# Kernel optimization log

Measured on AMD Instinct MI355X. Metric: run time of the kernel, lower is better.

The kernel has to match this reference:

```python
import jax, jax.numpy as jnp
import numpy as np
from jax import lax

EPS = 1e-5
KH, KW, PAD, DIL = 3, 3, 1, 1


def _bilinear_gather(x, py, px):
    """x: [B,C,H,W]; py/px: [B,K,H,W] float sample coords. Returns [B,C,K,H,W].
    Zero-padding semantics (torchvision deform_conv2d): corners outside the image contribute 0."""
    B, C, H, W = x.shape
    K = py.shape[1]
    y0 = jnp.floor(py)
    x0 = jnp.floor(px)
    wy1 = py - y0
    wy0 = 1.0 - wy1
    wx1 = px - x0
    wx0 = 1.0 - wx1
    xf = x.reshape(B, C, H * W)

    def corner(yc, xc, w):
        valid = (yc >= 0) & (yc <= H - 1) & (xc >= 0) & (xc <= W - 1)
        yi = jnp.clip(yc, 0, H - 1).astype(jnp.int32)
        xi = jnp.clip(xc, 0, W - 1).astype(jnp.int32)
        lin = (yi * W + xi).reshape(B, -1)  # [B, K*H*W]
        v = jax.vmap(lambda xb, lb: xb[:, lb])(xf, lin)  # [B, C, K*H*W]
        return v * (w * valid.astype(x.dtype)).reshape(B, 1, -1)

    out = (corner(y0, x0, wy0 * wx0)
           + corner(y0, x0 + 1.0, wy0 * wx1)
           + corner(y0 + 1.0, x0, wy1 * wx0)
           + corner(y0 + 1.0, x0 + 1.0, wy1 * wx1))
    return out.reshape(B, C, K, H, W)


def _deform_conv(x, offset, w):
    B, C, H, W = x.shape
    K = KH * KW
    off = offset.reshape(B, K, 2, H, W)  # (dy, dx) per kernel tap
    ki = (jnp.arange(K) // KW - PAD).astype(x.dtype)  # kernel row offset (dil=1)
    kj = (jnp.arange(K) % KW - PAD).astype(x.dtype)
    hh = jnp.arange(H).astype(x.dtype)
    ww = jnp.arange(W).astype(x.dtype)
    py = hh[None, None, :, None] + ki[None, :, None, None] + off[:, :, 0]
    px = ww[None, None, None, :] + kj[None, :, None, None] + off[:, :, 1]
    val = _bilinear_gather(x, py, px)  # [B,C,K,H,W]
    return jnp.einsum('bckhw,ock->bohw', val, w.reshape(w.shape[0], C, K))


def _bn(x, gamma, beta, mean, var):
    inv = gamma * lax.rsqrt(var + EPS)
    return x * inv[None, :, None, None] + (beta - mean * inv)[None, :, None, None]


def setup_inputs() -> dict:
    key = jax.random.key(0)
    ks = jax.random.split(key, 12)
    B, C, H, W = 4, 128, 128, 128
    return {
        'x': jax.random.normal(ks[0], (B, C, H, W), jnp.float32),
        'offset': jax.random.normal(ks[1], (B, 2 * KH * KW, H, W), jnp.float32),
        'w1': jax.random.normal(ks[2], (C, C, KH, KW), jnp.float32) * 0.05,
        'bn1_gamma': jax.random.uniform(ks[3], (C,), jnp.float32, 0.5, 1.5),
        'bn1_beta': jax.random.normal(ks[4], (C,), jnp.float32) * 0.1,
        'bn1_mean': jax.random.normal(ks[5], (C,), jnp.float32) * 0.1,
        'bn1_var': jax.random.uniform(ks[6], (C,), jnp.float32, 0.5, 1.5),
        'w2': jax.random.normal(ks[7], (C, C, KH, KW), jnp.float32) * 0.05,
        'bn2_gamma': jax.random.uniform(ks[8], (C,), jnp.float32, 0.5, 1.5),
        'bn2_beta': jax.random.normal(ks[9], (C,), jnp.float32) * 0.1,
        'bn2_mean': jax.random.normal(ks[10], (C,), jnp.float32) * 0.1,
        'bn2_var': jax.random.uniform(ks[11], (C,), jnp.float32, 0.5, 1.5),
    }


def reference(x, offset, w1, bn1_gamma, bn1_beta, bn1_mean, bn1_var,
              w2, bn2_gamma, bn2_beta, bn2_mean, bn2_var):
    identity = x
    out = _deform_conv(x, offset, w1)
    out = jax.nn.relu(_bn(out, bn1_gamma, bn1_beta, bn1_mean, bn1_var))
    out = lax.conv_general_dilated(out, w2, window_strides=(1, 1),
                                   padding=((PAD, PAD), (PAD, PAD)),
                                   dimension_numbers=('NCHW', 'OIHW', 'NCHW'))
    out = _bn(out, bn2_gamma, bn2_beta, bn2_mean, bn2_var)
    out = jax.nn.relu(out + identity)
    return out
```

## Files before the change

### kernel.cpp

```cpp
#include <hip/hip_runtime.h>
#include <hip/hip_fp16.h>
#include <stdint.h>

#define B_ 4
#define C_ 128
#define H_ 128
#define W_ 128
#define HW 16384

typedef _Float16 h8 __attribute__((ext_vector_type(8)));
typedef float f32x16 __attribute__((ext_vector_type(16)));

__device__ __forceinline__ unsigned cvtpk_f16(float lo, float hi) {
    auto r = __builtin_amdgcn_cvt_pkrtz(lo, hi);
    return *(unsigned*)&r;
}

__device__ __forceinline__ unsigned blend_h2(unsigned c0, unsigned c1, unsigned c2, unsigned c3,
                                             __half2 G0, __half2 G1, __half2 G2, __half2 G3) {
    __half2 s = __hmul2(G0, *(__half2*)&c0);
    s = __hfma2(G1, *(__half2*)&c1, s);
    s = __hfma2(G2, *(__half2*)&c2, s);
    s = __hfma2(G3, *(__half2*)&c3, s);
    return *(unsigned*)&s;
}

__device__ __forceinline__ void gll16(const void* g, void* l) {
    __builtin_amdgcn_global_load_lds((const unsigned int*)g, (unsigned int*)l, 16, 0, 0);
}

__global__ __launch_bounds__(256) void prep_all(const float* __restrict__ w1,
                                                const float* __restrict__ w2,
                                                unsigned short* __restrict__ w1f,
                                                unsigned short* __restrict__ w2t,
                                                unsigned short* __restrict__ o1p,
                                                const float* g1, const float* b1, const float* m1, const float* v1,
                                                const float* g2, const float* b2, const float* m2, const float* v2,
                                                float* inv1, float* sh1, float* inv2, float* sh2) {
    int blk = blockIdx.x;
    int tid = threadIdx.x;
    if (blk < 1152) {
        int i = blk * 256 + tid;
        if (i < 147456) {
            int o = i / 1152, rem = i % 1152;
            int c = rem / 9, tap = rem % 9;
            _Float16 hv = (_Float16)w1[i];
            int s = o >> 5;
            int ks = c >> 4;
            int l = (o & 31) | (((c >> 3) & 1) << 5);
            int jj = c & 7;
            w1f[(((tap * 4 + s) * 8 + ks) * 64 + l) * 8 + jj] = *(unsigned short*)&hv;
        } else {
            int j = i - 147456;
            int o = j / 1152, rem = j % 1152;
            int c = rem / 9, tap = rem % 9;
            _Float16 hv = (_Float16)w2[j];
            w2t[o * 1152 + tap * 128 + c] = *(unsigned short*)&hv;
        }
    } else if (blk < 1281) {
        int i = (blk - 1152) * 256 + tid;
        if (i < 33024) {
            int chunk = i & 15;
            int pos = i >> 4;
            int b = pos / 516;
            int r = pos % 516;
            int row, col;
            if (r < 130)      { row = 0;   col = r; }
            else if (r < 260) { row = 129; col = r - 130; }
            else { int j = r - 260; row = 1 + (j >> 1); col = (j & 1) * 129; }
            uint4 z = {0u, 0u, 0u, 0u};
            *(uint4*)((char*)o1p + (size_t)((b * 130 + row) * 130 + col) * 256 + chunk * 16) = z;
        }
    } else {
        if (tid < 128) {
            float iv = g1[tid] * rsqrtf(v1[tid] + 1e-5f);
            inv1[tid] = iv; sh1[tid] = b1[tid] - m1[tid] * iv;
        } else {
            int u = tid - 128;
            float iv = g2[u] * rsqrtf(v2[u] + 1e-5f);
            inv2[u] = iv; sh2[u] = b2[u] - m2[u] * iv;
        }
    }
}

__global__ __launch_bounds__(256) void nhwc_k(const float* __restrict__ x,
                                              unsigned short* __restrict__ xh) {
    __shared__ unsigned short tile[32][36];
    int blk = blockIdx.x;
    int wt = blk & 3, ct = (blk >> 2) & 3, h = (blk >> 4) & 127, b = blk >> 11;
    int t = threadIdx.x;
    int c = t >> 3, seg = t & 7;
    const float* srcp = x + ((size_t)((b * 128 + ct * 32 + c) * 128 + h) * 128) + wt * 32 + seg * 4;
    float4 v = *(const float4*)srcp;
    uint2 pk;
    pk.x = cvtpk_f16(v.x, v.y);
    pk.y = cvtpk_f16(v.z, v.w);
    *(uint2*)&tile[c][seg * 4] = pk;
    __syncthreads();
    int w = t >> 3, s2 = t & 7;
    unsigned a0 = tile[s2 * 4 + 0][w];
    unsigned a1 = tile[s2 * 4 + 1][w];
    unsigned a2 = tile[s2 * 4 + 2][w];
    unsigned a3 = tile[s2 * 4 + 3][w];
    uint2 o;
    o.x = (a1 << 16) | a0;
    o.y = (a3 << 16) | a2;
    *(uint2*)(xh + ((size_t)((b * 128 + h) * 128 + wt * 32 + w) * 128) + ct * 32 + s2 * 4) = o;
}

__global__ __launch_bounds__(512, 4) void gemm1_k(
    const unsigned short* __restrict__ xh,
    const float* __restrict__ off,
    const unsigned short* __restrict__ w1f,
    const float* __restrict__ inv1,
    const float* __restrict__ sh1,
    unsigned short* __restrict__ out1p) {
    __shared__ __align__(16) char ldsv[2][16384];

    int bid = blockIdx.x;
    int swz = ((bid & 7) << 7) | (bid >> 3);
    int half = swz & 1, h = (swz >> 1) & 127, b = swz >> 8;
    int w0 = half * 64;
    int tid = threadIdx.x;
    int bH = b * H_;
    const char* xb8 = (const char*)xh;

    if (tid < 256) {
        int prow = tid >> 4;
        int seg = tid & 15;
        int sb = seg * 16;

        float dy[4], dx[4];
        unsigned PX[4][4];
        float g[4][4];
        uint4 buf[2][4];

#define OFFLOAD(TT) do { \
    int dyB_ = ((b * 18 + 2 * (TT)) * H_ + h) * W_ + w0; \
    _Pragma("unroll") \
    for (int c_ = 0; c_ < 4; ++c_) { \
        int p_ = prow + c_ * 16; \
        dy[c_] = off[dyB_ + p_]; \
        dx[c_] = off[dyB_ + HW + p_]; \
    } \
} while (0)

#define COORD(TT) do { \
    int kh_ = (TT) / 3 - 1, kw_ = (TT) % 3 - 1; \
    _Pragma("unroll") \
    for (int c_ = 0; c_ < 4; ++c_) { \
        int p_ = prow + c_ * 16; \
        float py_ = (float)(h + kh_) + dy[c_]; \
        float px_ = (float)(w0 + p_ + kw_) + dx[c_]; \
        float y0f_ = floorf(py_), x0f_ = floorf(px_); \
        int y0_ = (int)y0f_, x0_ = (int)x0f_; \
        float wy1_ = py_ - y0f_, wx1_ = px_ - x0f_; \
        float wy0_ = 1.f - wy1_, wx0_ = 1.f - wx1_; \
        int y1_ = y0_ + 1, x1_ = x0_ + 1; \
        g[c_][0] = ((unsigned)y0_ < 128u && (unsigned)x0_ < 128u) ? wy0_ * wx0_ : 0.f; \
        g[c_][1] = ((unsigned)y0_ < 128u && (unsigned)x1_ < 128u) ? wy0_ * wx1_ : 0.f; \
        g[c_][2] = ((unsigned)y1_ < 128u && (unsigned)x0_ < 128u) ? wy1_ * wx0_ : 0.f; \
        g[c_][3] = ((unsigned)y1_ < 128u && (unsigned)x1_ < 128u) ? wy1_ * wx1_ : 0.f; \
        int y0c_ = min(max(y0_, 0), 127), y1c_ = min(max(y1_, 0), 127); \
        int x0c_ = min(max(x0_, 0), 127), x1c_ = min(max(x1_, 0), 127); \
        int r0_ = (bH + y0c_) * W_, r1_ = (bH + y1c_) * W_; \
        PX[c_][0] = (unsigned)((r0_ + x0c_) * 256) + sb; \
        PX[c_][1] = (unsigned)((r0_ + x1c_) * 256) + sb; \
        PX[c_][2] = (unsigned)((r1_ + x0c_) * 256) + sb; \
        PX[c_][3] = (unsigned)((r1_ + x1c_) * 256) + sb; \
    } \
} while (0)

#define ISSUE2(cA, cB) do { \
    _Pragma("unroll") \
    for (int k_ = 0; k_ < 4; ++k_) buf[0][k_] = *(const uint4*)(xb8 + PX[cA][k_]); \
    _Pragma("unroll") \
    for (int k_ = 0; k_ < 4; ++k_) buf[1][k_] = *(const uint4*)(xb8 + PX[cB][k_]); \
} while (0)

#define BLEND1(VP, CC, BI) do { \
    __half2 G0_ = __float2half2_rn(g[CC][0]); \
    __half2 G1_ = __float2half2_rn(g[CC][1]); \
    __half2 G2_ = __float2half2_rn(g[CC][2]); \
    __half2 G3_ = __float2half2_rn(g[CC][3]); \
    uint4 st_; \
    st_.x = blend_h2(buf[BI][0].x, buf[BI][1].x, buf[BI][2].x, buf[BI][3].x, G0_, G1_, G2_, G3_); \
    st_.y = blend_h2(buf[BI][0].y, buf[BI][1].y, buf[BI][2].y, buf[BI][3].y, G0_, G1_, G2_, G3_); \
    st_.z = blend_h2(buf[BI][0].z, buf[BI][1].z, buf[BI][2].z, buf[BI][3].z, G0_, G1_, G2_, G3_); \
    st_.w = blend_h2(buf[BI][0].w, buf[BI][1].w, buf[BI][2].w, buf[BI][3].w, G0_, G1_, G2_, G3_); \
    int row_ = prow + (CC) * 16; \
    *(uint4*)(&ldsv[VP][0] + row_ * 256 + ((seg ^ (row_ & 15)) << 4)) = st_; \
} while (0)

#define GATHER(VP) do { \
    ISSUE2(0, 1); \
    BLEND1(VP, 0, 0); BLEND1(VP, 1, 1); \
    ISSUE2(2, 3); \
    BLEND1(VP, 2, 0); BLEND1(VP, 3, 1); \
} while (0)

        OFFLOAD(0);
        COORD(0);
        GATHER(0);
        OFFLOAD(1);
        __syncthreads();
        for (int t = 0; t < 9; ++t) {
            if (t < 8) {
                COORD(t + 1);
                GATHER((t + 1) & 1);
                if (t < 7) OFFLOAD(t + 2);
            }
            __syncthreads();
        }
#undef OFFLOAD
#undef COORD
#undef ISSUE2
#undef BLEND1
#undef GATHER
    } else {
        int ctid = tid - 256;
        int lane = ctid & 63, wv2 = ctid >> 6;
        int wo = wv2 >> 1, wp = wv2 & 1;
        int lp = lane & 31, hi = lane >> 5;
        int bRow = (wp * 32 + lp) * 256;
        int lsw = lp & 15;

        f32x16 acc0 = {};
        f32x16 acc1 = {};

        __syncthreads();
        for (int t = 0; t < 9; ++t) {
            const unsigned short* wb = w1f + (t * 4 + 2 * wo) * 4096 + lane * 8;
            const char* vcur = &ldsv[t & 1][0];
            #pragma unroll 2
            for (int ks = 0; ks < 8; ++ks) {
                h8 a0 = *(const h8*)(wb + ks * 512);
                h8 a1 = *(const h8*)(wb + 4096 + ks * 512);
                int q0 = 2 * ks + hi;
                h8 bb = *(const h8*)(vcur + bRow + ((q0 ^ lsw) << 4));
                acc0 = __builtin_amdgcn_mfma_f32_32x32x16_f16(a0, bb, acc0, 0, 0, 0);
                acc1 = __builtin_amdgcn_mfma_f32_32x32x16_f16(a1, bb, acc1, 0, 0, 0);
            }
            __syncthreads();
        }

        int p = w0 + wp * 32 + lp;
        size_t rowbase = (size_t)((b * 130 + h + 1) * 130 + 1 + p) * 128;
        #pragma unroll
        for (int t = 0; t < 2; ++t) {
            #pragma unroll
            for (int k = 0; k < 4; ++k) {
                int o0 = wo * 64 + t * 32 + k * 8 + hi * 4;
                float4 iv = *(const float4*)(inv1 + o0);
                float4 sv = *(const float4*)(sh1 + o0);
                float e0, e1, e2, e3;
                if (t == 0) {
                    e0 = acc0[4 * k + 0]; e1 = acc0[4 * k + 1];
                    e2 = acc0[4 * k + 2]; e3 = acc0[4 * k + 3];
                } else {
                    e0 = acc1[4 * k + 0]; e1 = acc1[4 * k + 1];
                    e2 = acc1[4 * k + 2]; e3 = acc1[4 * k + 3];
                }
                float v0 = fmaxf(fmaf(e0, iv.x, sv.x), 0.f);
                float v1 = fmaxf(fmaf(e1, iv.y, sv.y), 0.f);
                float v2 = fmaxf(fmaf(e2, iv.z, sv.z), 0.f);
                float v3 = fmaxf(fmaf(e3, iv.w, sv.w), 0.f);
                uint2 pk2;
                pk2.x = cvtpk_f16(v0, v1);
                pk2.y = cvtpk_f16(v2, v3);
                *(uint2*)(out1p + rowbase + o0) = pk2;
            }
        }
    }
}

__global__ __launch_bounds__(512, 4) void gemm2_k(
    const unsigned short* __restrict__ out1p,
    const unsigned short* __restrict__ w2t,
    const unsigned short* __restrict__ xh,
    const float* __restrict__ inv2,
    const float* __restrict__ sh2,
    float* __restrict__ outp) {
    __shared__ __align__(16) char ldsS[33280];
    __shared__ __align__(16) char ldsw[32768];

    int bid = blockIdx.x;
    int swz = ((bid & 7) << 6) | (bid >> 3);
    int h = swz & 127, b = swz >> 7;
    int tid = threadIdx.x, lane = tid & 63, wv = tid >> 6;
    int wo = wv >> 2, wp = wv & 3;
    int lp = lane & 31, hi = lane >> 5;

    f32x16 acc0 = {};
    f32x16 acc1 = {};

    int aRow0 = (wo * 64 + lp) * 256;
    int aRow1 = aRow0 + 32 * 256;
    int lsw = lp & 15;

    for (int kh = 0; kh < 3; ++kh) {
        __syncthreads();
        const char* srow = (const char*)out1p + (size_t)((b * 130 + h + kh) * 130) * 256;
        #pragma unroll
        for (int it = 0; it < 5; ++it) {
            int ci = it * 512 + tid;
            if (ci < 2080) {
                int r = ci >> 4, q = ci & 15;
                gll16(srow + r * 256 + ((q ^ (r & 15)) << 4), ldsS + ci * 16);
            }
        }
        for (int kw = 0; kw < 3; ++kw) {
            if (kw) __syncthreads();
            int tap = kh * 3 + kw;
            #pragma unroll
            for (int it = 0; it < 4; ++it) {
                int ci = it * 512 + tid;
                int o = ci >> 4, q = ci & 15;
                gll16((const char*)w2t + o * 2304 + tap * 256 + ((q ^ (o & 15)) << 4), ldsw + ci * 16);
            }
            __syncthreads();
            int pr = (wp * 32 + lp + kw) * 256;
            int prw = (wp * 32 + lp + kw) & 15;
            #pragma unroll
            for (int ks = 0; ks < 8; ++ks) {
                int q0 = 2 * ks + hi;
                h8 bb = *(const h8*)(ldsS + pr + ((q0 ^ prw) << 4));
                int sl = (q0 ^ lsw) << 4;
                h8 a0 = *(const h8*)(ldsw + aRow0 + sl);
                h8 a1 = *(const h8*)(ldsw + aRow1 + sl);
                acc0 = __builtin_amdgcn_mfma_f32_32x32x16_f16(a0, bb, acc0, 0, 0, 0);
                acc1 = __builtin_amdgcn_mfma_f32_32x32x16_f16(a1, bb, acc1, 0, 0, 0);
            }
        }
    }

    int p = wp * 32 + lp;
    const unsigned short* xrow = xh + (size_t)((b * 128 + h) * 128 + p) * 128;
    #pragma unroll
    for (int t = 0; t < 2; ++t) {
        #pragma unroll
        for (int k = 0; k < 4; ++k) {
            int o0 = wo * 64 + t * 32 + k * 8 + hi * 4;
            uint2 rx = *(const uint2*)(xrow + o0);
            __half2 hx0 = *(__half2*)&rx.x;
            __half2 hx1 = *(__half2*)&rx.y;
            float x0 = __low2float(hx0), x1 = __high2float(hx0);
            float x2 = __low2float(hx1), x3 = __high2float(hx1);
            float e0, e1, e2, e3;
            if (t == 0) {
                e0 = acc0[4 * k + 0]; e1 = acc0[4 * k + 1];
                e2 = acc0[4 * k + 2]; e3 = acc0[4 * k + 3];
            } else {
                e0 = acc1[4 * k + 0]; e1 = acc1[4 * k + 1];
                e2 = acc1[4 * k + 2]; e3 = acc1[4 * k + 3];
            }
            size_t idx = ((size_t)(b * C_ + o0) * H_ + h) * W_ + p;
            outp[idx]            = fmaxf(fmaf(e0, inv2[o0 + 0], sh2[o0 + 0]) + x0, 0.f);
            outp[idx + HW]       = fmaxf(fmaf(e1, inv2[o0 + 1], sh2[o0 + 1]) + x1, 0.f);
            outp[idx + 2 * HW]   = fmaxf(fmaf(e2, inv2[o0 + 2], sh2[o0 + 2]) + x2, 0.f);
            outp[idx + 3 * HW]   = fmaxf(fmaf(e3, inv2[o0 + 3], sh2[o0 + 3]) + x3, 0.f);
        }
    }
}

extern "C" void kernel_launch(void* const* d_in, const int* in_sizes, int n_in,
                              void* d_out, int out_size, void* d_ws, size_t ws_size,
                              hipStream_t stream) {
    const float* x   = (const float*)d_in[0];
    const float* off = (const float*)d_in[1];
    const float* w1  = (const float*)d_in[2];
    const float* g1  = (const float*)d_in[3];
    const float* b1  = (const float*)d_in[4];
    const float* m1  = (const float*)d_in[5];
    const float* v1  = (const float*)d_in[6];
    const float* w2  = (const float*)d_in[7];
    const float* g2  = (const float*)d_in[8];
    const float* b2  = (const float*)d_in[9];
    const float* m2  = (const float*)d_in[10];
    const float* v2  = (const float*)d_in[11];
    float* outp = (float*)d_out;

    char* ws = (char*)d_ws;
    unsigned short* w1f = (unsigned short*)(ws);
    unsigned short* w2t = (unsigned short*)(ws + 294912);
    float* inv1 = (float*)(ws + 589824);
    float* sh1  = (float*)(ws + 590336);
    float* inv2 = (float*)(ws + 590848);
    float* sh2  = (float*)(ws + 591360);
    unsigned short* xh  = (unsigned short*)(ws + 591872);
    unsigned short* o1p = (unsigned short*)(ws + 17369088);

    prep_all<<<1282, 256, 0, stream>>>(w1, w2, w1f, w2t, o1p,
                                       g1, b1, m1, v1, g2, b2, m2, v2,
                                       inv1, sh1, inv2, sh2);
    nhwc_k<<<8192, 256, 0, stream>>>(x, xh);
    gemm1_k<<<1024, 512, 0, stream>>>(xh, off, w1f, inv1, sh1, o1p);
    gemm2_k<<<512, 512, 0, stream>>>(o1p, w2t, xh, inv2, sh2, outp);
}
```

Baseline: 102.1 us.

## Merge NHWC conversion into prep kernel and register-prefetch weights in gemm1 MFMA warps

```diff
diff --git a/kernel.cpp b/kernel.cpp
--- a/kernel.cpp
+++ b/kernel.cpp
@@ -29,7 +29,9 @@
     __builtin_amdgcn_global_load_lds((const unsigned int*)g, (unsigned int*)l, 16, 0, 0);
 }
 
-__global__ __launch_bounds__(256) void prep_all(const float* __restrict__ w1,
+__global__ __launch_bounds__(256) void prep_all(const float* __restrict__ x,
+                                                unsigned short* __restrict__ xh,
+                                                const float* __restrict__ w1,
                                                 const float* __restrict__ w2,
                                                 unsigned short* __restrict__ w1f,
                                                 unsigned short* __restrict__ w2t,
@@ -37,8 +39,31 @@
                                                 const float* g1, const float* b1, const float* m1, const float* v1,
                                                 const float* g2, const float* b2, const float* m2, const float* v2,
                                                 float* inv1, float* sh1, float* inv2, float* sh2) {
+    __shared__ unsigned short tile[32][36];
     int blk = blockIdx.x;
     int tid = threadIdx.x;
+    if (blk >= 1282) {
+        int nb = blk - 1282;
+        int wt = nb & 3, ct = (nb >> 2) & 3, h = (nb >> 4) & 127, b = nb >> 11;
+        int c = tid >> 3, seg = tid & 7;
+        const float* srcp = x + ((size_t)((b * 128 + ct * 32 + c) * 128 + h) * 128) + wt * 32 + seg * 4;
+        float4 v = *(const float4*)srcp;
+        uint2 pk;
+        pk.x = cvtpk_f16(v.x, v.y);
+        pk.y = cvtpk_f16(v.z, v.w);
+        *(uint2*)&tile[c][seg * 4] = pk;
+        __syncthreads();
+        int w = tid >> 3, s2 = tid & 7;
+        unsigned a0 = tile[s2 * 4 + 0][w];
+        unsigned a1 = tile[s2 * 4 + 1][w];
+        unsigned a2 = tile[s2 * 4 + 2][w];
+        unsigned a3 = tile[s2 * 4 + 3][w];
+        uint2 o;
+        o.x = (a1 << 16) | a0;
+        o.y = (a3 << 16) | a2;
+        *(uint2*)(xh + ((size_t)((b * 128 + h) * 128 + wt * 32 + w) * 128) + ct * 32 + s2 * 4) = o;
+        return;
+    }
     if (blk < 1152) {
         int i = blk * 256 + tid;
         if (i < 147456) {
@@ -81,31 +106,6 @@
             inv2[u] = iv; sh2[u] = b2[u] - m2[u] * iv;
         }
     }
-}
-
-__global__ __launch_bounds__(256) void nhwc_k(const float* __restrict__ x,
-                                              unsigned short* __restrict__ xh) {
-    __shared__ unsigned short tile[32][36];
-    int blk = blockIdx.x;
-    int wt = blk & 3, ct = (blk >> 2) & 3, h = (blk >> 4) & 127, b = blk >> 11;
-    int t = threadIdx.x;
-    int c = t >> 3, seg = t & 7;
-    const float* srcp = x + ((size_t)((b * 128 + ct * 32 + c) * 128 + h) * 128) + wt * 32 + seg * 4;
-    float4 v = *(const float4*)srcp;
-    uint2 pk;
-    pk.x = cvtpk_f16(v.x, v.y);
-    pk.y = cvtpk_f16(v.z, v.w);
-    *(uint2*)&tile[c][seg * 4] = pk;
-    __syncthreads();
-    int w = t >> 3, s2 = t & 7;
-    unsigned a0 = tile[s2 * 4 + 0][w];
-    unsigned a1 = tile[s2 * 4 + 1][w];
-    unsigned a2 = tile[s2 * 4 + 2][w];
-    unsigned a3 = tile[s2 * 4 + 3][w];
-    uint2 o;
-    o.x = (a1 << 16) | a0;
-    o.y = (a3 << 16) | a2;
-    *(uint2*)(xh + ((size_t)((b * 128 + h) * 128 + wt * 32 + w) * 128) + ct * 32 + s2 * 4) = o;
 }
 
 __global__ __launch_bounds__(512, 4) void gemm1_k(
@@ -219,42 +219,54 @@
 #undef GATHER
     } else {
         int ctid = tid - 256;
-        int lane = ctid & 63, wv2 = ctid >> 6;
-        int wo = wv2 >> 1, wp = wv2 & 1;
+        int lane = ctid & 63, wq = ctid >> 6;
         int lp = lane & 31, hi = lane >> 5;
-        int bRow = (wp * 32 + lp) * 256;
         int lsw = lp & 15;
+        int bRow0 = lp * 256;
+        int bRow1 = (32 + lp) * 256;
 
         f32x16 acc0 = {};
         f32x16 acc1 = {};
-
+        h8 wreg[2][8];
+
+        {
+            const unsigned short* wb = w1f + wq * 4096 + lane * 8;
+            #pragma unroll
+            for (int ks = 0; ks < 8; ++ks) wreg[0][ks] = *(const h8*)(wb + ks * 512);
+        }
         __syncthreads();
+        #pragma unroll
         for (int t = 0; t < 9; ++t) {
-            const unsigned short* wb = w1f + (t * 4 + 2 * wo) * 4096 + lane * 8;
+            if (t < 8) {
+                const unsigned short* wb = w1f + ((t + 1) * 4 + wq) * 4096 + lane * 8;
+                #pragma unroll
+                for (int ks = 0; ks < 8; ++ks) wreg[(t + 1) & 1][ks] = *(const h8*)(wb + ks * 512);
+            }
             const char* vcur = &ldsv[t & 1][0];
-            #pragma unroll 2
+            #pragma unroll
             for (int ks = 0; ks < 8; ++ks) {
-                h8 a0 = *(const h8*)(wb + ks * 512);
-                h8 a1 = *(const h8*)(wb + 4096 + ks * 512);
                 int q0 = 2 * ks + hi;
-                h8 bb = *(const h8*)(vcur + bRow + ((q0 ^ lsw) << 4));
-                acc0 = __builtin_amdgcn_mfma_f32_32x32x16_f16(a0, bb, acc0, 0, 0, 0);
-                acc1 = __builtin_amdgcn_mfma_f32_32x32x16_f16(a1, bb, acc1, 0, 0, 0);
+                int sl = (q0 ^ lsw) << 4;
+                h8 b0 = *(const h8*)(vcur + bRow0 + sl);
+                h8 b1 = *(const h8*)(vcur + bRow1 + sl);
+                h8 a = wreg[t & 1][ks];
+                acc0 = __builtin_amdgcn_mfma_f32_32x32x16_f16(a, b0, acc0, 0, 0, 0);
+                acc1 = __builtin_amdgcn_mfma_f32_32x32x16_f16(a, b1, acc1, 0, 0, 0);
             }
             __syncthreads();
         }
 
-        int p = w0 + wp * 32 + lp;
-        size_t rowbase = (size_t)((b * 130 + h + 1) * 130 + 1 + p) * 128;
         #pragma unroll
-        for (int t = 0; t < 2; ++t) {
+        for (int j = 0; j < 2; ++j) {
+            int p = w0 + j * 32 + lp;
+            size_t rowbase = (size_t)((b * 130 + h + 1) * 130 + 1 + p) * 128;
             #pragma unroll
             for (int k = 0; k < 4; ++k) {
-                int o0 = wo * 64 + t * 32 + k * 8 + hi * 4;
+                int o0 = wq * 32 + k * 8 + hi * 4;
                 float4 iv = *(const float4*)(inv1 + o0);
                 float4 sv = *(const float4*)(sh1 + o0);
                 float e0, e1, e2, e3;
-                if (t == 0) {
+                if (j == 0) {
                     e0 = acc0[4 * k + 0]; e1 = acc0[4 * k + 1];
                     e2 = acc0[4 * k + 2]; e3 = acc0[4 * k + 3];
                 } else {
@@ -390,10 +402,9 @@
     unsigned short* xh  = (unsigned short*)(ws + 591872);
     unsigned short* o1p = (unsigned short*)(ws + 17369088);
 
-    prep_all<<<1282, 256, 0, stream>>>(w1, w2, w1f, w2t, o1p,
+    prep_all<<<9474, 256, 0, stream>>>(x, xh, w1, w2, w1f, w2t, o1p,
                                        g1, b1, m1, v1, g2, b2, m2, v2,
                                        inv1, sh1, inv2, sh2);
-    nhwc_k<<<8192, 256, 0, stream>>>(x, xh);
     gemm1_k<<<1024, 512, 0, stream>>>(xh, off, w1f, inv1, sh1, o1p);
     gemm2_k<<<512, 512, 0, stream>>>(o1p, w2t, xh, inv2, sh2, outp);
 }
```

Result: faster. 87.25 us (-14.5%).
